# Performance work log

Hardware: AMD Instinct MI355X
Metric: run time of the kernel (lower is better)

## Reference

```python
import jax, jax.numpy as jnp
import numpy as np

B, H, W = 4, 704, 704
M, P, NN, R = 32, 128, 129, 1
GAIN = 2.0


def setup_inputs() -> dict:
    key = jax.random.key(0)
    ks = jax.random.split(key, 10)
    # reference boxes: (x,y,z, w,h,d, yaw) -- sizes must be positive (log / divide)
    ref_xyz = jax.random.normal(ks[0], (B, M, 3)) * 10.0
    ref_whd = jax.random.uniform(ks[1], (B, M, 3), minval=0.8, maxval=3.0)
    ref_yaw = jax.random.uniform(ks[2], (B, M, 1), minval=-3.1, maxval=3.1)
    ref_boxes = jnp.concatenate([ref_xyz, ref_whd, ref_yaw], axis=-1)
    pred_class = jax.random.normal(ks[3], (B, 4, H, W))
    pred_regress = jax.random.normal(ks[4], (B, 14, H, W)) * 0.1
    # anchor grid [2 anchors, 7 box params, H, W]; sizes positive
    a_xyz = jax.random.normal(ks[5], (2, 3, H, W))
    a_whd = jax.random.uniform(ks[6], (2, 3, H, W), minval=0.8, maxval=3.0)
    a_yaw = jnp.concatenate([jnp.zeros((1, 1, H, W)), jnp.full((1, 1, H, W), jnp.pi / 2)], axis=0)
    anchor = jnp.concatenate([a_xyz, a_whd, a_yaw], axis=1)
    pos_idx = jax.random.randint(ks[7], (B, P, 2), 0, H)
    neg_idx = jax.random.randint(ks[8], (B, NN, 2), 0, H)
    reg_idx = jax.random.randint(ks[9], (B, M, R, 2), 0, H)
    return {"ref_boxes": ref_boxes, "pred_class": pred_class, "pred_regress": pred_regress,
            "anchor": anchor, "pos_idx": pos_idx, "neg_idx": neg_idx, "reg_idx": reg_idx}


def _smooth_l1(d):
    a = jnp.abs(d)
    return jnp.where(a < 1.0, 0.5 * d * d, a - 0.5)


def _ce_mean(logits, label_idx):
    # CrossEntropyLoss(mean) with constant label = label_idx for every row
    return -jax.nn.log_softmax(logits, axis=-1)[:, label_idx].mean()


def reference(ref_boxes, pred_class, pred_regress, anchor, pos_idx, neg_idx, reg_idx):
    def per_batch(rb, pc, pr, pidx, nidx, ridx):
        # ---- classification: two anchors, pos label=1 / neg label=0 ----
        pos_logits = pc[:, pidx[:, 0], pidx[:, 1]]   # [4, P]
        neg_logits = pc[:, nidx[:, 0], nidx[:, 1]]   # [4, NN]
        cls = 0.0
        for a0 in (0, 2):  # predicted_class_feature[:2] then [2:4]
            cls = cls + _ce_mean(pos_logits[a0:a0 + 2].T, 1) + _ce_mean(neg_logits[a0:a0 + 2].T, 0)
        px, py = ridx[..., 0], ridx[..., 1]                       # [M, R]
        pbox = jnp.transpose(pr[:, px, py], (1, 2, 0)).reshape(M, R, 2, 7)   # [M,R,2,7]
        abox = jnp.transpose(anchor[:, :, px, py], (2, 3, 0, 1))             # [M,R,2,7]
        ref = rb[:, None, None, :]                                            # [M,1,1,7]
        diag = jnp.sqrt(abox[..., 3] ** 2 + abox[..., 4] ** 2)
        xy = (ref[..., :2] - abox[..., :2]) / diag[..., None]
        z = (ref[..., 2:3] - abox[..., 2:3]) / abox[..., 5:6]
        whd = jnp.log(ref[..., 3:6] / abox[..., 3:6])
        dth = ref[..., 6] - abox[..., 6]
        ori = jnp.arctan2(jnp.sin(dth), jnp.cos(dth))[..., None]
        off = jnp.concatenate([xy, z, whd, ori], axis=-1)        # [M,R,2,7]
        reg = _smooth_l1(pbox - off).mean(axis=(1, 2, 3)).sum()  # per-box mean, sum over boxes
        return cls + GAIN * reg

    losses = jax.vmap(per_batch)(ref_boxes, pred_class, pred_regress, pos_idx, neg_idx, reg_idx)
    # original overwrites total_loss each batch iteration -> last batch's loss survives
    return losses[-1]
```

## Files before the change

kernel.cpp:

```cpp
#include <hip/hip_runtime.h>
#include <math.h>

#define BB 4
#define HH 704
#define WW 704
#define MM 32
#define PP 128
#define NNEG 129
#define RR 1
#define GAIN 2.0f
#define HW (HH * WW)


#define NTHREADS 640
#define NWAVES (NTHREADS / 64)

__global__ __launch_bounds__(NTHREADS) void loss_total_kernel(
    const float* __restrict__ rb,
    const float* __restrict__ pc,
    const float* __restrict__ pr,
    const float* __restrict__ anchor,
    const int* __restrict__ pidx,
    const int* __restrict__ nidx,
    const int* __restrict__ ridx,
    float* __restrict__ out)
{
    const int tid = threadIdx.x;
    const int b = BB - 1;

    const float* rb_b   = rb + (size_t)b * MM * 7;
    const float* pc_b   = pc + (size_t)b * 4 * HW;
    const float* pr_b   = pr + (size_t)b * 14 * HW;
    const int2*  pidx_b = (const int2*)(pidx + (size_t)b * PP * 2);
    const int2*  nidx_b = (const int2*)(nidx + (size_t)b * NNEG * 2);
    const int2*  ridx_b = (const int2*)(ridx + (size_t)b * MM * RR * 2);

    float acc = 0.0f;

    if (tid < 514) {
        int a0, scol;
        float inv_n;
        int2 yx;
        if (tid < 256) {
            a0   = (tid >> 7) * 2;
            yx   = pidx_b[tid & 127];
            scol = 1;
            inv_n = 1.0f / PP;
        } else {
            int j = tid - 256;
            a0   = (j / NNEG) * 2;
            yx   = nidx_b[j % NNEG];
            scol = 0;
            inv_n = 1.0f / NNEG;
        }
        size_t pix = (size_t)yx.x * WW + yx.y;
        float l0 = pc_b[(size_t)a0       * HW + pix];
        float l1 = pc_b[(size_t)(a0 + 1) * HW + pix];
        float mx  = fmaxf(l0, l1);
        float lse = mx + logf(expf(l0 - mx) + expf(l1 - mx));
        float lbl = scol ? l1 : l0;
        acc = (lse - lbl) * inv_n;
    } else if (tid < 578) {
        int k = tid - 514;
        int a = k & 1;
        int m = k >> 1;
        int2 yx = ridx_b[m];
        size_t pix = (size_t)yx.x * WW + yx.y;

        float ab[7], pb[7], rf[7];
        #pragma unroll
        for (int c = 0; c < 7; ++c) {
            ab[c] = anchor[(size_t)(a * 7 + c) * HW + pix];
            pb[c] = pr_b  [(size_t)(a * 7 + c) * HW + pix];
            rf[c] = rb_b[m * 7 + c];
        }

        float diag = sqrtf(ab[3] * ab[3] + ab[4] * ab[4]);
        float off[7];
        off[0] = (rf[0] - ab[0]) / diag;
        off[1] = (rf[1] - ab[1]) / diag;
        off[2] = (rf[2] - ab[2]) / ab[5];
        off[3] = logf(rf[3] / ab[3]);
        off[4] = logf(rf[4] / ab[4]);
        off[5] = logf(rf[5] / ab[5]);
        float dth = rf[6] - ab[6];
        off[6] = atan2f(sinf(dth), cosf(dth));

        float s = 0.0f;
        #pragma unroll
        for (int c = 0; c < 7; ++c) {
            float d = pb[c] - off[c];
            float ad = fabsf(d);
            s += (ad < 1.0f) ? 0.5f * d * d : (ad - 0.5f);
        }
        acc = s * (GAIN / (float)(RR * 2 * 7));
    }

    #pragma unroll
    for (int off = 32; off > 0; off >>= 1)
        acc += __shfl_down(acc, off, 64);

    __shared__ float wsum[NWAVES];
    int wave = tid >> 6;
    int lane = tid & 63;
    if (lane == 0) wsum[wave] = acc;
    __syncthreads();
    if (tid == 0) {
        float t = 0.0f;
        #pragma unroll
        for (int w = 0; w < NWAVES; ++w) t += wsum[w];
        out[0] = t;
    }
}

extern "C" void kernel_launch(void* const* d_in, const int* in_sizes, int n_in,
                              void* d_out, int out_size, void* d_ws, size_t ws_size,
                              hipStream_t stream) {
    const float* rb     = (const float*)d_in[0];
    const float* pc     = (const float*)d_in[1];
    const float* pr     = (const float*)d_in[2];
    const float* anchor = (const float*)d_in[3];
    const int*   pidx   = (const int*)d_in[4];
    const int*   nidx   = (const int*)d_in[5];
    const int*   ridx   = (const int*)d_in[6];
    float* out = (float*)d_out;

    loss_total_kernel<<<1, NTHREADS, 0, stream>>>(rb, pc, pr, anchor, pidx, nidx, ridx, out);
}
```

Before: 175.6 us.

## Split loss over ten single-wave blocks with a separate final reduction kernel

Replaces the single 640-thread block with ten 64-thread blocks, each writing a wave-reduced partial sum to workspace. A second single-thread kernel then sums the ten partials. The goal is to spread the scattered gathers across several compute units instead of one. In exchange it adds a second kernel launch and a global-memory round trip for the partials.

```diff
diff --git a/kernel.cpp b/kernel.cpp
--- a/kernel.cpp
+++ b/kernel.cpp
@@ -12,10 +12,10 @@
 #define HW (HH * WW)
 
 
-#define NTHREADS 640
-#define NWAVES (NTHREADS / 64)
+#define BLOCK 64
+#define NBLOCKS 10
 
-__global__ __launch_bounds__(NTHREADS) void loss_total_kernel(
+__global__ __launch_bounds__(BLOCK) void loss_partial_kernel(
     const float* __restrict__ rb,
     const float* __restrict__ pc,
     const float* __restrict__ pr,
@@ -23,9 +23,9 @@
     const int* __restrict__ pidx,
     const int* __restrict__ nidx,
     const int* __restrict__ ridx,
-    float* __restrict__ out)
+    float* __restrict__ partial)
 {
-    const int tid = threadIdx.x;
+    const int g = blockIdx.x * BLOCK + threadIdx.x;
     const int b = BB - 1;
 
     const float* rb_b   = rb + (size_t)b * MM * 7;
@@ -37,17 +37,17 @@
 
     float acc = 0.0f;
 
-    if (tid < 514) {
+    if (g < 514) {
         int a0, scol;
         float inv_n;
         int2 yx;
-        if (tid < 256) {
-            a0   = (tid >> 7) * 2;
-            yx   = pidx_b[tid & 127];
+        if (g < 256) {
+            a0   = (g >> 7) * 2;
+            yx   = pidx_b[g & 127];
             scol = 1;
             inv_n = 1.0f / PP;
         } else {
-            int j = tid - 256;
+            int j = g - 256;
             a0   = (j / NNEG) * 2;
             yx   = nidx_b[j % NNEG];
             scol = 0;
@@ -60,8 +60,8 @@
         float lse = mx + logf(expf(l0 - mx) + expf(l1 - mx));
         float lbl = scol ? l1 : l0;
         acc = (lse - lbl) * inv_n;
-    } else if (tid < 578) {
-        int k = tid - 514;
+    } else if (g < 578) {
+        int k = g - 514;
         int a = k & 1;
         int m = k >> 1;
         int2 yx = ridx_b[m];
@@ -100,15 +100,17 @@
     for (int off = 32; off > 0; off >>= 1)
         acc += __shfl_down(acc, off, 64);
 
-    __shared__ float wsum[NWAVES];
-    int wave = tid >> 6;
-    int lane = tid & 63;
-    if (lane == 0) wsum[wave] = acc;
-    __syncthreads();
-    if (tid == 0) {
+    if (threadIdx.x == 0) partial[blockIdx.x] = acc;
+}
+
+__global__ __launch_bounds__(64) void loss_final_kernel(
+    const float* __restrict__ partial,
+    float* __restrict__ out)
+{
+    if (threadIdx.x == 0) {
         float t = 0.0f;
         #pragma unroll
-        for (int w = 0; w < NWAVES; ++w) t += wsum[w];
+        for (int w = 0; w < NBLOCKS; ++w) t += partial[w];
         out[0] = t;
     }
 }
@@ -124,6 +126,9 @@
     const int*   nidx   = (const int*)d_in[5];
     const int*   ridx   = (const int*)d_in[6];
     float* out = (float*)d_out;
+    float* partial = (float*)d_ws;
 
-    loss_total_kernel<<<1, NTHREADS, 0, stream>>>(rb, pc, pr, anchor, pidx, nidx, ridx, out);
+    loss_partial_kernel<<<NBLOCKS, BLOCK, 0, stream>>>(
+        rb, pc, pr, anchor, pidx, nidx, ridx, partial);
+    loss_final_kernel<<<1, 64, 0, stream>>>(partial, out);
 }
```

Result: no change. 173.9 us (-0.9%).
